# Optimization experiments

Measured on AMD Instinct MI355X. Metric: run time of the kernel, lower is better.

The kernel has to match this reference:

```python
import jax, jax.numpy as jnp
import numpy as np

B = 2048       # number of samples
A = 64         # max agents per sample (static)
E = 128        # h_dim
H = 8          # num_heads
DH = E // H    # head dim = 16


def _agents():
    # deterministic ragged pattern covering 1..64; sum = 66560
    return jnp.asarray(((np.arange(B) * 7) % A) + 1, dtype=jnp.int32)


def setup_inputs() -> dict:
    key = jax.random.key(0)
    ks = jax.random.split(key, 6)
    agents = _agents()
    total = int(np.sum(((np.arange(B) * 7) % A) + 1))  # 66560
    att_in = jax.random.normal(ks[0], (total, E), dtype=jnp.float32)
    # nn.MultiheadAttention parameters
    in_proj_w = jax.random.normal(ks[1], (3 * E, E), dtype=jnp.float32) * 0.02
    in_proj_b = jnp.zeros((3 * E,), dtype=jnp.float32)
    out_proj_w = jax.random.normal(ks[2], (E, E), dtype=jnp.float32) * 0.02
    out_proj_b = jnp.zeros((E,), dtype=jnp.float32)
    return {
        "att_in": att_in,
        "in_proj_w": in_proj_w,
        "in_proj_b": in_proj_b,
        "out_proj_w": out_proj_w,
        "out_proj_b": out_proj_b,
        "agents_per_sample": agents,
    }


def reference(att_in, in_proj_w, in_proj_b, out_proj_w, out_proj_b, agents_per_sample):
    total = att_in.shape[0]
    # ---- pad ragged [total, E] -> [B, A, E] ----
    sample_ids = jnp.repeat(jnp.arange(B), agents_per_sample, total_repeat_length=total)
    offsets = jnp.concatenate([jnp.zeros((1,), jnp.int32), jnp.cumsum(agents_per_sample)[:-1]])
    slot_ids = jnp.arange(total) - offsets[sample_ids]
    padded = jnp.zeros((B, A, E), att_in.dtype).at[sample_ids, slot_ids].set(att_in)
    key_valid = jnp.arange(A)[None, :] < agents_per_sample[:, None]  # [B, A]

    # ---- multi-head self-attention (dropout disabled / eval mode) ----
    qkv = padded @ in_proj_w.T + in_proj_b            # [B, A, 3E]
    q, k, v = jnp.split(qkv, 3, axis=-1)
    def heads(x):
        return x.reshape(B, A, H, DH).transpose(0, 2, 1, 3)  # [B, H, A, DH]
    q, k, v = heads(q), heads(k), heads(v)
    scores = jnp.einsum("bhqd,bhkd->bhqk", q, k) / jnp.sqrt(jnp.float32(DH))
    scores = jnp.where(key_valid[:, None, None, :], scores, jnp.float32(-1e9))
    attn = jax.nn.softmax(scores, axis=-1)            # [B, H, A, A]
    ctx = jnp.einsum("bhqk,bhkd->bhqd", attn, v)      # [B, H, A, DH]
    ctx = ctx.transpose(0, 2, 1, 3).reshape(B, A, E)
    out = ctx @ out_proj_w.T + out_proj_b             # [B, A, E]

    # ---- unpad back to flat ragged [total, E] ----
    return out[sample_ids, slot_ids]
```

## Files before the change

kernel.cpp:

```cpp
#include <hip/hip_runtime.h>

#define NB    2048
#define AMAX  64
#define EDIM  128
#define TOTAL 66560
#define DHEAD 16
#define KVSTR 20
#define XSTR  129
#define LSTR  136
#define WELEM 65536

typedef _Float16 f16x8 __attribute__((ext_vector_type(8)));
typedef _Float16 f16x4 __attribute__((ext_vector_type(4)));
typedef float    f32x4 __attribute__((ext_vector_type(4)));

__global__ __launch_bounds__(256) void prep_kernel(const int* __restrict__ ag,
                                                   int* __restrict__ offs,
                                                   const float* __restrict__ win,
                                                   const float* __restrict__ wout,
                                                   _Float16* __restrict__ wh) {
    if (blockIdx.x == 0) {
        __shared__ int part[256];
        const int t = threadIdx.x;
        int loc[8];
        int s = 0;
#pragma unroll
        for (int i = 0; i < 8; ++i) { loc[i] = s; s += ag[t * 8 + i]; }
        part[t] = s;
        __syncthreads();
        for (int d = 1; d < 256; d <<= 1) {
            int v = (t >= d) ? part[t - d] : 0;
            __syncthreads();
            part[t] += v;
            __syncthreads();
        }
        const int base = (t == 0) ? 0 : part[t - 1];
#pragma unroll
        for (int i = 0; i < 8; ++i) offs[t * 8 + i] = base + loc[i];
    } else {
        const int base = (blockIdx.x - 1) * 1024 + threadIdx.x * 4;
        const float4 v = (base < 49152) ? *(const float4*)(win + base)
                                        : *(const float4*)(wout + (base - 49152));
        f16x4 h;
        h[0] = (_Float16)v.x; h[1] = (_Float16)v.y;
        h[2] = (_Float16)v.z; h[3] = (_Float16)v.w;
        *(f16x4*)(wh + base) = h;
    }
}

__global__ __launch_bounds__(256, 2) void fused_attn_kernel(
    const float*    __restrict__ x,
    const _Float16* __restrict__ winh,
    const float*    __restrict__ bin,
    const _Float16* __restrict__ woh,
    const float*    __restrict__ bout,
    const int*      __restrict__ ag,
    const int*      __restrict__ offs,
    float*          __restrict__ out)
{
    __shared__ __align__(16) _Float16 xs[AMAX * LSTR];

    const int i    = blockIdx.x;
    const int b    = (((63 - (i >> 5)) * 55) & 63) + ((i & 31) << 6);
    const int n    = ag[b];
    const int off  = offs[b];
    const int tid  = threadIdx.x;
    const int lane = tid & 63;
    const int wid  = __builtin_amdgcn_readfirstlane(tid >> 6);
    const int l15  = lane & 15;
    const int quad = lane >> 4;
    const int nt   = (n + 15) >> 4;

    f16x8 wq[2][4], wk[2][4], wv[2][4];
    float bqa[2][4], bka[2][4], bva[2];
#pragma unroll
    for (int m = 0; m < 2; ++m) {
        const int h = wid * 2 + m;
#pragma unroll
        for (int ks = 0; ks < 4; ++ks) {
            wq[m][ks] = *(const f16x8*)(winh + (size_t)(h * 16 + l15) * EDIM + ks * 32 + quad * 8);
            wk[m][ks] = *(const f16x8*)(winh + (size_t)(128 + h * 16 + l15) * EDIM + ks * 32 + quad * 8);
            wv[m][ks] = *(const f16x8*)(winh + (size_t)(256 + h * 16 + l15) * EDIM + ks * 32 + quad * 8);
        }
        const float4 bq = *(const float4*)(bin + h * 16 + quad * 4);
        const float4 bk = *(const float4*)(bin + 128 + h * 16 + quad * 4);
        bqa[m][0]=bq.x; bqa[m][1]=bq.y; bqa[m][2]=bq.z; bqa[m][3]=bq.w;
        bka[m][0]=bk.x; bka[m][1]=bk.y; bka[m][2]=bk.z; bka[m][3]=bk.w;
        bva[m] = bin[256 + h * 16 + l15];
    }

#pragma unroll
    for (int it = 0; it < 4; ++it) if (it < nt) {
        const int u = it * 256 + tid;
        const int r = u >> 4, c8 = u & 15;
        f16x8 hv = {};
        if (r < n) {
            const float4 a0 = *(const float4*)(x + (size_t)(off + r) * EDIM + c8 * 8);
            const float4 a1 = *(const float4*)(x + (size_t)(off + r) * EDIM + c8 * 8 + 4);
            hv[0]=(_Float16)a0.x; hv[1]=(_Float16)a0.y; hv[2]=(_Float16)a0.z; hv[3]=(_Float16)a0.w;
            hv[4]=(_Float16)a1.x; hv[5]=(_Float16)a1.y; hv[6]=(_Float16)a1.z; hv[7]=(_Float16)a1.w;
        }
        *(f16x8*)(xs + r * LSTR + c8 * 8) = hv;
    }
    __syncthreads();

    const float QSC = 0.25f * 1.44269504088896f;
    f16x4 qf[2][4], kf[2][4], vf[2][4];
#pragma unroll
    for (int kt = 0; kt < 4; ++kt) if (kt < nt) {
        f16x8 xf[4];
#pragma unroll
        for (int ks = 0; ks < 4; ++ks)
            xf[ks] = *(const f16x8*)(xs + (kt * 16 + l15) * LSTR + ks * 32 + quad * 8);
#pragma unroll
        for (int m = 0; m < 2; ++m) {
            f32x4 aq = (f32x4){0.f,0.f,0.f,0.f};
            f32x4 ak = (f32x4){0.f,0.f,0.f,0.f};
            f32x4 av = (f32x4){0.f,0.f,0.f,0.f};
#pragma unroll
            for (int ks = 0; ks < 4; ++ks) {
                aq = __builtin_amdgcn_mfma_f32_16x16x32_f16(wq[m][ks], xf[ks], aq, 0, 0, 0);
                ak = __builtin_amdgcn_mfma_f32_16x16x32_f16(wk[m][ks], xf[ks], ak, 0, 0, 0);
                av = __builtin_amdgcn_mfma_f32_16x16x32_f16(xf[ks], wv[m][ks], av, 0, 0, 0);
            }
#pragma unroll
            for (int r = 0; r < 4; ++r) {
                qf[m][kt][r] = (_Float16)((aq[r] + bqa[m][r]) * QSC);
                kf[m][kt][r] = (_Float16)(ak[r] + bka[m][r]);
                vf[m][kt][r] = (_Float16)(av[r] + bva[m]);
            }
        }
    }

    f16x4 ctxf[2][4] = {};
#pragma unroll
    for (int qt = 0; qt < 4; ++qt) if (qt < nt) {
        f32x4 sv0[4], sv1[4];
#pragma unroll
        for (int kt = 0; kt < 4; ++kt) if (kt < nt) {
            sv0[kt] = __builtin_amdgcn_mfma_f32_16x16x16f16(
                          kf[0][kt], qf[0][qt], (f32x4){0.f,0.f,0.f,0.f}, 0, 0, 0);
            sv1[kt] = __builtin_amdgcn_mfma_f32_16x16x16f16(
                          kf[1][kt], qf[1][qt], (f32x4){0.f,0.f,0.f,0.f}, 0, 0, 0);
        }
        float t0[4], t1[4];
#pragma unroll
        for (int kt = 0; kt < 4; ++kt) { t0[kt] = 0.f; t1[kt] = 0.f; }
#pragma unroll
        for (int kt = 0; kt < 4; ++kt) if (kt < nt) {
            float s0 = 0.f, s1 = 0.f;
#pragma unroll
            for (int r = 0; r < 4; ++r) {
                const int key = kt * 16 + quad * 4 + r;
                const float p0 = (key < n) ? __builtin_amdgcn_exp2f(sv0[kt][r]) : 0.f;
                const float p1 = (key < n) ? __builtin_amdgcn_exp2f(sv1[kt][r]) : 0.f;
                s0 += p0; sv0[kt][r] = p0;
                s1 += p1; sv1[kt][r] = p1;
            }
            t0[kt] = s0; t1[kt] = s1;
        }
        float ls0 = (t0[0] + t0[1]) + (t0[2] + t0[3]);
        float ls1 = (t1[0] + t1[1]) + (t1[2] + t1[3]);
        ls0 += __shfl_xor(ls0, 16, 64);
        ls1 += __shfl_xor(ls1, 16, 64);
        ls0 += __shfl_xor(ls0, 32, 64);
        ls1 += __shfl_xor(ls1, 32, 64);
        const float inv0 = __builtin_amdgcn_rcpf(ls0);
        const float inv1 = __builtin_amdgcn_rcpf(ls1);
        f16x4 pf0[4], pf1[4];
#pragma unroll
        for (int kt = 0; kt < 4; ++kt) if (kt < nt) {
#pragma unroll
            for (int r = 0; r < 4; ++r) {
                pf0[kt][r] = (_Float16)(sv0[kt][r] * inv0);
                pf1[kt][r] = (_Float16)(sv1[kt][r] * inv1);
            }
        }
        f32x4 a0A = (f32x4){0.f,0.f,0.f,0.f}, a0B = (f32x4){0.f,0.f,0.f,0.f};
        f32x4 a1A = (f32x4){0.f,0.f,0.f,0.f}, a1B = (f32x4){0.f,0.f,0.f,0.f};
#pragma unroll
        for (int kt = 0; kt < 4; ++kt) if (kt < nt) {
            if ((kt & 1) == 0) {
                a0A = __builtin_amdgcn_mfma_f32_16x16x16f16(pf0[kt], vf[0][kt], a0A, 0, 0, 0);
                a1A = __builtin_amdgcn_mfma_f32_16x16x16f16(pf1[kt], vf[1][kt], a1A, 0, 0, 0);
            } else {
                a0B = __builtin_amdgcn_mfma_f32_16x16x16f16(pf0[kt], vf[0][kt], a0B, 0, 0, 0);
                a1B = __builtin_amdgcn_mfma_f32_16x16x16f16(pf1[kt], vf[1][kt], a1B, 0, 0, 0);
            }
        }
#pragma unroll
        for (int r = 0; r < 4; ++r) {
            ctxf[0][qt][r] = (_Float16)(a0A[r] + a0B[r]);
            ctxf[1][qt][r] = (_Float16)(a1A[r] + a1B[r]);
        }
    }

    __syncthreads();
#pragma unroll
    for (int m = 0; m < 2; ++m) {
        const int h = wid * 2 + m;
#pragma unroll
        for (int qt = 0; qt < 4; ++qt) if (qt < nt) {
#pragma unroll
            for (int r = 0; r < 4; ++r)
                xs[(qt * 16 + quad * 4 + r) * LSTR + h * 16 + l15] = ctxf[m][qt][r];
        }
    }
    __syncthreads();

    {
        f32x4 oacc[4][2];
#pragma unroll
        for (int t = 0; t < 4; ++t) { oacc[t][0] = (f32x4){0.f,0.f,0.f,0.f}; oacc[t][1] = (f32x4){0.f,0.f,0.f,0.f}; }
#pragma unroll
        for (int ks = 0; ks < 4; ++ks) {
            f16x8 cf[2];
#pragma unroll
            for (int c2 = 0; c2 < 2; ++c2)
                cf[c2] = *(const f16x8*)(woh + (wid * 32 + c2 * 16 + l15) * EDIM + ks * 32 + quad * 8);
#pragma unroll
            for (int t = 0; t < 4; ++t) if (t < nt) {
                const f16x8 rf = *(const f16x8*)(xs + (t * 16 + l15) * LSTR + ks * 32 + quad * 8);
                oacc[t][0] = __builtin_amdgcn_mfma_f32_16x16x32_f16(cf[0], rf, oacc[t][0], 0, 0, 0);
                oacc[t][1] = __builtin_amdgcn_mfma_f32_16x16x32_f16(cf[1], rf, oacc[t][1], 0, 0, 0);
            }
        }
        const float4 bo0 = *(const float4*)(bout + wid * 32 + quad * 4);
        const float4 bo1 = *(const float4*)(bout + wid * 32 + 16 + quad * 4);
#pragma unroll
        for (int t = 0; t < 4; ++t) if (t < nt) {
            const int row = t * 16 + l15;
            if (row < n) {
                float* orow = out + (size_t)(off + row) * EDIM + wid * 32;
                *(float4*)(orow + quad * 4) =
                    make_float4(oacc[t][0][0] + bo0.x, oacc[t][0][1] + bo0.y,
                                oacc[t][0][2] + bo0.z, oacc[t][0][3] + bo0.w);
                *(float4*)(orow + 16 + quad * 4) =
                    make_float4(oacc[t][1][0] + bo1.x, oacc[t][1][1] + bo1.y,
                                oacc[t][1][2] + bo1.z, oacc[t][1][3] + bo1.w);
            }
        }
    }
}

__global__ __launch_bounds__(256, 2) void attn_fused_kernel(
    const float* __restrict__ x, const float* __restrict__ win,
    const float* __restrict__ bin, const float* __restrict__ wout,
    const float* __restrict__ bout, const int* __restrict__ ag,
    const int* __restrict__ offs, float* __restrict__ out)
{
    __shared__ __align__(16) float xs[AMAX * XSTR];
    __shared__ __align__(16) float kvs[8][AMAX * KVSTR];
    const int b = blockIdx.x, n = ag[b], off = offs[b];
    const int tid = threadIdx.x, lane = tid & 63;
    const int wid = __builtin_amdgcn_readfirstlane(tid >> 6);
#pragma unroll
    for (int it = 0; it < 8; ++it) {
        const int f4 = it * 256 + tid;
        const int r = f4 >> 5, c = (f4 & 31) << 2;
        float4 v = make_float4(0.f, 0.f, 0.f, 0.f);
        if (r < n) v = *(const float4*)(x + (size_t)(off + r) * EDIM + c);
        float* d = xs + r * XSTR + c;
        d[0]=v.x; d[1]=v.y; d[2]=v.z; d[3]=v.w;
    }
    __syncthreads();
    float* kw = kvs[wid*2+0]; float* vw = kvs[wid*2+1];
    const float* xrow = xs + lane * XSTR;
    float ctxk[2][DHEAD];
#pragma unroll
    for (int m = 0; m < 2; ++m) {
        const int h = wid * 2 + m;
        float qa[DHEAD], ka[DHEAD], va[DHEAD];
#pragma unroll
        for (int d = 0; d < DHEAD; ++d) { qa[d]=0.f; ka[d]=0.f; va[d]=0.f; }
        const float* wq = win + (size_t)(h*DHEAD)*EDIM;
        const float* wk = win + (size_t)(EDIM + h*DHEAD)*EDIM;
        const float* wv = win + (size_t)(2*EDIM + h*DHEAD)*EDIM;
        for (int k = 0; k < EDIM; ++k) {
            const float xv = xrow[k];
#pragma unroll
            for (int d = 0; d < DHEAD; ++d) {
                qa[d] = fmaf(xv, wq[d*EDIM+k], qa[d]);
                ka[d] = fmaf(xv, wk[d*EDIM+k], ka[d]);
                va[d] = fmaf(xv, wv[d*EDIM+k], va[d]);
            }
        }
#pragma unroll
        for (int d = 0; d < DHEAD; ++d) {
            qa[d] = (qa[d] + bin[h*DHEAD+d]) * 0.25f;
            ka[d] += bin[EDIM + h*DHEAD + d];
            va[d] += bin[2*EDIM + h*DHEAD + d];
        }
#pragma unroll
        for (int d = 0; d < DHEAD; ++d) { kw[lane*KVSTR+d] = ka[d]; vw[lane*KVSTR+d] = va[d]; }
        float mrun = -1e30f, lrun = 0.f, cacc[DHEAD];
#pragma unroll
        for (int d = 0; d < DHEAD; ++d) cacc[d] = 0.f;
        const int nch = (n + 15) >> 4;
        for (int ch = 0; ch < nch; ++ch) {
            const int jb = ch << 4;
            float s[16], p[16];
#pragma unroll
            for (int jj = 0; jj < 16; ++jj) {
                const float4* kr = (const float4*)(kw + (jb + jj) * KVSTR);
                const float4 k0=kr[0],k1=kr[1],k2=kr[2],k3=kr[3];
                const float kk[16] = {k0.x,k0.y,k0.z,k0.w,k1.x,k1.y,k1.z,k1.w,
                                      k2.x,k2.y,k2.z,k2.w,k3.x,k3.y,k3.z,k3.w};
                float a = 0.f;
#pragma unroll
                for (int d = 0; d < DHEAD; ++d) a = fmaf(qa[d], kk[d], a);
                s[jj] = (jb + jj < n) ? a : -1e30f;
            }
            float mc = s[0];
#pragma unroll
            for (int jj = 1; jj < 16; ++jj) mc = fmaxf(mc, s[jj]);
            const float mnew = fmaxf(mrun, mc);
            const float alpha = __expf(mrun - mnew);
            float psum = 0.f;
#pragma unroll
            for (int jj = 0; jj < 16; ++jj) { p[jj] = __expf(s[jj]-mnew); psum += p[jj]; }
            lrun = fmaf(lrun, alpha, psum);
#pragma unroll
            for (int d = 0; d < DHEAD; ++d) cacc[d] *= alpha;
#pragma unroll
            for (int jj = 0; jj < 16; ++jj) {
                const float4* vr = (const float4*)(vw + (jb + jj) * KVSTR);
                const float4 v0=vr[0],v1=vr[1],v2=vr[2],v3=vr[3];
                const float vv[16] = {v0.x,v0.y,v0.z,v0.w,v1.x,v1.y,v1.z,v1.w,
                                      v2.x,v2.y,v2.z,v2.w,v3.x,v3.y,v3.z,v3.w};
                const float pj = p[jj];
#pragma unroll
                for (int d = 0; d < DHEAD; ++d) cacc[d] = fmaf(pj, vv[d], cacc[d]);
            }
            mrun = mnew;
        }
        const float inv = 1.0f / lrun;
#pragma unroll
        for (int d = 0; d < DHEAD; ++d) ctxk[m][d] = cacc[d] * inv;
    }
    __syncthreads();
#pragma unroll
    for (int m = 0; m < 2; ++m) {
        const int h = wid * 2 + m;
#pragma unroll
        for (int d = 0; d < DHEAD; ++d) xs[lane*XSTR + h*DHEAD + d] = ctxk[m][d];
    }
    __syncthreads();
    const int c0 = wid * 32;
#pragma unroll
    for (int ct = 0; ct < 4; ++ct) {
        const int cc = c0 + ct * 8;
        float a8[8];
#pragma unroll
        for (int j = 0; j < 8; ++j) a8[j] = 0.f;
#pragma unroll 4
        for (int e = 0; e < EDIM; ++e) {
            const float cv = xrow[e];
#pragma unroll
            for (int j = 0; j < 8; ++j) a8[j] = fmaf(cv, wout[(size_t)(cc+j)*EDIM+e], a8[j]);
        }
        if (lane < n) {
            float* orow = out + (size_t)(off + lane) * EDIM + cc;
#pragma unroll
            for (int j = 0; j < 8; ++j) orow[j] = a8[j] + bout[cc+j];
        }
    }
}

extern "C" void kernel_launch(void* const* d_in, const int* in_sizes, int n_in,
                              void* d_out, int out_size, void* d_ws, size_t ws_size,
                              hipStream_t stream) {
    const float* x   = (const float*)d_in[0];
    const float* win = (const float*)d_in[1];
    const float* bin = (const float*)d_in[2];
    const float* wo  = (const float*)d_in[3];
    const float* bo  = (const float*)d_in[4];
    const int*   ag  = (const int*)d_in[5];
    float* out = (float*)d_out;

    const size_t need = (size_t)WELEM * sizeof(_Float16) + NB * sizeof(int);
    if (ws_size >= need) {
        _Float16* wh = (_Float16*)d_ws;
        int* offs = (int*)(wh + WELEM);
        prep_kernel<<<65, 256, 0, stream>>>(ag, offs, win, wo, wh);
        fused_attn_kernel<<<NB, 256, 0, stream>>>(x, wh, bin, wh + 49152, bo, ag, offs, out);
    } else {
        int* offs = (int*)d_ws;
        prep_kernel<<<1, 256, 0, stream>>>(ag, offs, nullptr, nullptr, nullptr);
        attn_fused_kernel<<<NB, 256, 0, stream>>>(x, win, bin, wo, bo, ag, offs, out);
    }
}
```

Measured before the change: 138.2 us.

## Pack multiple small samples into one block via 16-row tile descriptors

The prep kernel now bins samples by tile count (nt = 1..4) and builds a descriptor table that packs several short samples into one 64-row block (3+1, 2+2, 1+1+1+1, etc.). The attention kernel reads four tile descriptors per block and masks cross-sample score tiles by comparing sample ids. Blocks past the computed count exit early. This cuts the number of mostly-empty blocks and their wasted projection work, in exchange for a more complex single-thread packing step in prep and always running the full four-tile projection MFMAs.

Measured after the change: 128.5 us, median of 2. 1.08x faster.

```diff
diff --git a/kernel.cpp b/kernel.cpp
--- a/kernel.cpp
+++ b/kernel.cpp
@@ -9,6 +9,7 @@
 #define XSTR  129
 #define LSTR  136
 #define WELEM 65536
+#define NSLOT 8192
 
 typedef _Float16 f16x8 __attribute__((ext_vector_type(8)));
 typedef _Float16 f16x4 __attribute__((ext_vector_type(4)));
@@ -18,14 +19,19 @@
                                                    int* __restrict__ offs,
                                                    const float* __restrict__ win,
                                                    const float* __restrict__ wout,
-                                                   _Float16* __restrict__ wh) {
+                                                   _Float16* __restrict__ wh,
+                                                   int4* __restrict__ dsc,
+                                                   int* __restrict__ nblk) {
     if (blockIdx.x == 0) {
         __shared__ int part[256];
+        __shared__ int cnt[8];
+        __shared__ int rk[8];
+        __shared__ int cb[8];
         const int t = threadIdx.x;
-        int loc[8];
+        int myn[8], loc[8];
         int s = 0;
 #pragma unroll
-        for (int i = 0; i < 8; ++i) { loc[i] = s; s += ag[t * 8 + i]; }
+        for (int i = 0; i < 8; ++i) { myn[i] = ag[t * 8 + i]; loc[i] = s; s += myn[i]; }
         part[t] = s;
         __syncthreads();
         for (int d = 1; d < 256; d <<= 1) {
@@ -37,6 +43,53 @@
         const int base = (t == 0) ? 0 : part[t - 1];
 #pragma unroll
         for (int i = 0; i < 8; ++i) offs[t * 8 + i] = base + loc[i];
+
+        if (dsc != nullptr) {
+            for (int j = t; j < NSLOT; j += 256)
+                dsc[j] = make_int4(0, 0, -(j + 1), j & 3);
+            if (t < 8) { cnt[t] = 0; rk[t] = 0; }
+            __syncthreads();
+#pragma unroll
+            for (int i = 0; i < 8; ++i)
+                atomicAdd(&cnt[(myn[i] + 15) >> 4], 1);
+            __syncthreads();
+            if (t == 0) {
+                const int c4 = cnt[4], c3 = cnt[3], c2 = cnt[2], c1 = cnt[1];
+                const int p31 = (c3 < c1) ? c3 : c1;
+                const int q2 = c2 >> 1, odd2 = c2 & 1;
+                int u1a = c1 - p31; const int cap = odd2 ? 2 : 0;
+                if (u1a > cap) u1a = cap; if (u1a < 0) u1a = 0;
+                const int rem1 = c1 - p31 - u1a;
+                cb[4] = 0; cb[3] = c4; cb[2] = c4 + c3;
+                cb[0] = p31; cb[1] = u1a;
+                nblk[0] = c4 + c3 + q2 + odd2 + ((rem1 + 3) >> 2);
+            }
+            __syncthreads();
+#pragma unroll
+            for (int i = 0; i < 8; ++i) {
+                const int sid = t * 8 + i, n = myn[i], off = base + loc[i];
+                const int nt = (n + 15) >> 4;
+                const int r = atomicAdd(&rk[nt], 1);
+                int blk, s0;
+                if (nt == 4)      { blk = r;            s0 = 0; }
+                else if (nt == 3) { blk = cb[3] + r;    s0 = 0; }
+                else if (nt == 2) { blk = cb[2] + (r >> 1); s0 = (r & 1) << 1; }
+                else {
+                    const int p31 = cb[0], u1a = cb[1], c2 = cnt[2];
+                    if (r < p31)            { blk = cb[3] + r;          s0 = 3; }
+                    else if (r < p31 + u1a) { blk = cb[2] + (c2 >> 1);  s0 = 2 + (r - p31); }
+                    else {
+                        const int rr = r - p31 - u1a;
+                        blk = cb[2] + (c2 >> 1) + (c2 & 1) + (rr >> 2);
+                        s0 = rr & 3;
+                    }
+                }
+                for (int tt = 0; tt < nt; ++tt) {
+                    int nrem = n - tt * 16; if (nrem > 16) nrem = 16;
+                    dsc[blk * 4 + s0 + tt] = make_int4(off + tt * 16, nrem, sid, s0 | (n << 8));
+                }
+            }
+        }
     } else {
         const int base = (blockIdx.x - 1) * 1024 + threadIdx.x * 4;
         const float4 v = (base < 49152) ? *(const float4*)(win + base)
@@ -54,22 +107,23 @@
     const float*    __restrict__ bin,
     const _Float16* __restrict__ woh,
     const float*    __restrict__ bout,
-    const int*      __restrict__ ag,
-    const int*      __restrict__ offs,
+    const int4*     __restrict__ dsc,
+    const int*      __restrict__ nblk,
     float*          __restrict__ out)
 {
     __shared__ __align__(16) _Float16 xs[AMAX * LSTR];
 
-    const int i    = blockIdx.x;
-    const int b    = (((63 - (i >> 5)) * 55) & 63) + ((i & 31) << 6);
-    const int n    = ag[b];
-    const int off  = offs[b];
+    const int b = blockIdx.x;
+    if (b >= nblk[0]) return;
     const int tid  = threadIdx.x;
     const int lane = tid & 63;
     const int wid  = __builtin_amdgcn_readfirstlane(tid >> 6);
     const int l15  = lane & 15;
     const int quad = lane >> 4;
-    const int nt   = (n + 15) >> 4;
+
+    int4 dd[4];
+#pragma unroll
+    for (int t = 0; t < 4; ++t) dd[t] = dsc[b * 4 + t];
 
     f16x8 wq[2][4], wk[2][4], wv[2][4];
     float bqa[2][4], bka[2][4], bva[2];
@@ -89,25 +143,27 @@
         bva[m] = bin[256 + h * 16 + l15];
     }
 
-#pragma unroll
-    for (int it = 0; it < 4; ++it) if (it < nt) {
-        const int u = it * 256 + tid;
-        const int r = u >> 4, c8 = u & 15;
-        f16x8 hv = {};
-        if (r < n) {
-            const float4 a0 = *(const float4*)(x + (size_t)(off + r) * EDIM + c8 * 8);
-            const float4 a1 = *(const float4*)(x + (size_t)(off + r) * EDIM + c8 * 8 + 4);
-            hv[0]=(_Float16)a0.x; hv[1]=(_Float16)a0.y; hv[2]=(_Float16)a0.z; hv[3]=(_Float16)a0.w;
-            hv[4]=(_Float16)a1.x; hv[5]=(_Float16)a1.y; hv[6]=(_Float16)a1.z; hv[7]=(_Float16)a1.w;
-        }
-        *(f16x8*)(xs + r * LSTR + c8 * 8) = hv;
+    {
+        const int rr = tid >> 4, c8 = tid & 15;
+#pragma unroll
+        for (int t = 0; t < 4; ++t) {
+            f16x8 hv = {};
+            if (rr < dd[t].y) {
+                const float* xr = x + (size_t)(dd[t].x + rr) * EDIM + c8 * 8;
+                const float4 a0 = *(const float4*)xr;
+                const float4 a1 = *(const float4*)(xr + 4);
+                hv[0]=(_Float16)a0.x; hv[1]=(_Float16)a0.y; hv[2]=(_Float16)a0.z; hv[3]=(_Float16)a0.w;
+                hv[4]=(_Float16)a1.x; hv[5]=(_Float16)a1.y; hv[6]=(_Float16)a1.z; hv[7]=(_Float16)a1.w;
+            }
+            *(f16x8*)(xs + (t * 16 + rr) * LSTR + c8 * 8) = hv;
+        }
     }
     __syncthreads();
 
     const float QSC = 0.25f * 1.44269504088896f;
     f16x4 qf[2][4], kf[2][4], vf[2][4];
 #pragma unroll
-    for (int kt = 0; kt < 4; ++kt) if (kt < nt) {
+    for (int kt = 0; kt < 4; ++kt) {
         f16x8 xf[4];
 #pragma unroll
         for (int ks = 0; ks < 4; ++ks)
@@ -134,10 +190,17 @@
 
     f16x4 ctxf[2][4] = {};
 #pragma unroll
-    for (int qt = 0; qt < 4; ++qt) if (qt < nt) {
+    for (int qt = 0; qt < 4; ++qt) {
+        const int baseq = dd[qt].w & 255;
+        const int nsq   = dd[qt].w >> 8;
+        const int sidq  = dd[qt].z;
+        bool act[4];
+#pragma unroll
+        for (int kt = 0; kt < 4; ++kt) act[kt] = (dd[kt].z == sidq);
+
         f32x4 sv0[4], sv1[4];
 #pragma unroll
-        for (int kt = 0; kt < 4; ++kt) if (kt < nt) {
+        for (int kt = 0; kt < 4; ++kt) if (act[kt]) {
             sv0[kt] = __builtin_amdgcn_mfma_f32_16x16x16f16(
                           kf[0][kt], qf[0][qt], (f32x4){0.f,0.f,0.f,0.f}, 0, 0, 0);
             sv1[kt] = __builtin_amdgcn_mfma_f32_16x16x16f16(
@@ -147,13 +210,13 @@
 #pragma unroll
         for (int kt = 0; kt < 4; ++kt) { t0[kt] = 0.f; t1[kt] = 0.f; }
 #pragma unroll
-        for (int kt = 0; kt < 4; ++kt) if (kt < nt) {
+        for (int kt = 0; kt < 4; ++kt) if (act[kt]) {
             float s0 = 0.f, s1 = 0.f;
 #pragma unroll
             for (int r = 0; r < 4; ++r) {
-                const int key = kt * 16 + quad * 4 + r;
-                const float p0 = (key < n) ? __builtin_amdgcn_exp2f(sv0[kt][r]) : 0.f;
-                const float p1 = (key < n) ? __builtin_amdgcn_exp2f(sv1[kt][r]) : 0.f;
+                const int key = (kt - baseq) * 16 + quad * 4 + r;
+                const float p0 = (key < nsq) ? __builtin_amdgcn_exp2f(sv0[kt][r]) : 0.f;
+                const float p1 = (key < nsq) ? __builtin_amdgcn_exp2f(sv1[kt][r]) : 0.f;
                 s0 += p0; sv0[kt][r] = p0;
                 s1 += p1; sv1[kt][r] = p1;
             }
@@ -169,7 +232,7 @@
         const float inv1 = __builtin_amdgcn_rcpf(ls1);
         f16x4 pf0[4], pf1[4];
 #pragma unroll
-        for (int kt = 0; kt < 4; ++kt) if (kt < nt) {
+        for (int kt = 0; kt < 4; ++kt) if (act[kt]) {
 #pragma unroll
             for (int r = 0; r < 4; ++r) {
                 pf0[kt][r] = (_Float16)(sv0[kt][r] * inv0);
@@ -179,7 +242,7 @@
         f32x4 a0A = (f32x4){0.f,0.f,0.f,0.f}, a0B = (f32x4){0.f,0.f,0.f,0.f};
         f32x4 a1A = (f32x4){0.f,0.f,0.f,0.f}, a1B = (f32x4){0.f,0.f,0.f,0.f};
 #pragma unroll
-        for (int kt = 0; kt < 4; ++kt) if (kt < nt) {
+        for (int kt = 0; kt < 4; ++kt) if (act[kt]) {
             if ((kt & 1) == 0) {
                 a0A = __builtin_amdgcn_mfma_f32_16x16x16f16(pf0[kt], vf[0][kt], a0A, 0, 0, 0);
                 a1A = __builtin_amdgcn_mfma_f32_16x16x16f16(pf1[kt], vf[1][kt], a1A, 0, 0, 0);
@@ -200,7 +263,7 @@
     for (int m = 0; m < 2; ++m) {
         const int h = wid * 2 + m;
 #pragma unroll
-        for (int qt = 0; qt < 4; ++qt) if (qt < nt) {
+        for (int qt = 0; qt < 4; ++qt) {
 #pragma unroll
             for (int r = 0; r < 4; ++r)
                 xs[(qt * 16 + quad * 4 + r) * LSTR + h * 16 + l15] = ctxf[m][qt][r];
@@ -219,7 +282,7 @@
             for (int c2 = 0; c2 < 2; ++c2)
                 cf[c2] = *(const f16x8*)(woh + (wid * 32 + c2 * 16 + l15) * EDIM + ks * 32 + quad * 8);
 #pragma unroll
-            for (int t = 0; t < 4; ++t) if (t < nt) {
+            for (int t = 0; t < 4; ++t) {
                 const f16x8 rf = *(const f16x8*)(xs + (t * 16 + l15) * LSTR + ks * 32 + quad * 8);
                 oacc[t][0] = __builtin_amdgcn_mfma_f32_16x16x32_f16(cf[0], rf, oacc[t][0], 0, 0, 0);
                 oacc[t][1] = __builtin_amdgcn_mfma_f32_16x16x32_f16(cf[1], rf, oacc[t][1], 0, 0, 0);
@@ -228,10 +291,9 @@
         const float4 bo0 = *(const float4*)(bout + wid * 32 + quad * 4);
         const float4 bo1 = *(const float4*)(bout + wid * 32 + 16 + quad * 4);
 #pragma unroll
-        for (int t = 0; t < 4; ++t) if (t < nt) {
-            const int row = t * 16 + l15;
-            if (row < n) {
-                float* orow = out + (size_t)(off + row) * EDIM + wid * 32;
+        for (int t = 0; t < 4; ++t) {
+            if (l15 < dd[t].y) {
+                float* orow = out + (size_t)(dd[t].x + l15) * EDIM + wid * 32;
                 *(float4*)(orow + quad * 4) =
                     make_float4(oacc[t][0][0] + bo0.x, oacc[t][0][1] + bo0.y,
                                 oacc[t][0][2] + bo0.z, oacc[t][0][3] + bo0.w);
@@ -378,15 +440,18 @@
     const int*   ag  = (const int*)d_in[5];
     float* out = (float*)d_out;
 
-    const size_t need = (size_t)WELEM * sizeof(_Float16) + NB * sizeof(int);
+    const size_t need = (size_t)WELEM * sizeof(_Float16) + (size_t)NSLOT * sizeof(int4)
+                      + NB * sizeof(int) + 4 * sizeof(int);
     if (ws_size >= need) {
         _Float16* wh = (_Float16*)d_ws;
-        int* offs = (int*)(wh + WELEM);
-        prep_kernel<<<65, 256, 0, stream>>>(ag, offs, win, wo, wh);
-        fused_attn_kernel<<<NB, 256, 0, stream>>>(x, wh, bin, wh + 49152, bo, ag, offs, out);
+        int4* dsc = (int4*)(wh + WELEM);
+        int* offs = (int*)(dsc + NSLOT);
+        int* nblk = offs + NB;
+        prep_kernel<<<65, 256, 0, stream>>>(ag, offs, win, wo, wh, dsc, nblk);
+        fused_attn_kernel<<<NB, 256, 0, stream>>>(x, wh, bin, wh + 49152, bo, dsc, nblk, out);
     } else {
         int* offs = (int*)d_ws;
-        prep_kernel<<<1, 256, 0, stream>>>(ag, offs, nullptr, nullptr, nullptr);
+        prep_kernel<<<1, 256, 0, stream>>>(ag, offs, nullptr, nullptr, nullptr, nullptr, nullptr);
         attn_fused_kernel<<<NB, 256, 0, stream>>>(x, win, bin, wo, bo, ag, offs, out);
     }
 }
```
